# Optimization experiments

Measured on AMD Instinct MI355X. Metric: run time of the kernel, lower is better.

Reference implementation:

```python
import jax, jax.numpy as jnp
import numpy as np

H = 1024
NH = 16
HD = H // NH  # 64


def setup_inputs() -> dict:
    key = jax.random.key(0)
    ks = jax.random.split(key, 8)
    B, S = 4, 1024
    scale = 1.0 / np.sqrt(H)
    return {
        "hidden_states": jax.random.normal(ks[0], (B, S, H), jnp.float32),
        "attention_mask": jnp.ones((B, S), jnp.float32),
        "Wq": jax.random.normal(ks[1], (H, H), jnp.float32) * scale,
        "bq": jnp.zeros((H,), jnp.float32),
        "Wk": jax.random.normal(ks[2], (H, H), jnp.float32) * scale,
        "bk": jnp.zeros((H,), jnp.float32),
        "Wv": jax.random.normal(ks[3], (H, H), jnp.float32) * scale,
        "bv": jnp.zeros((H,), jnp.float32),
        "Wo": jax.random.normal(ks[4], (H, H), jnp.float32) * scale,
        "bo": jnp.zeros((H,), jnp.float32),
    }


def _split_heads(x):
    # [B,S,H] -> [B,NH,S,HD]
    B, S, _ = x.shape
    return x.reshape(B, S, NH, HD).transpose(0, 2, 1, 3)


def reference(hidden_states, attention_mask, Wq, bq, Wk, bk, Wv, bv, Wo, bo):
    B, S, _ = hidden_states.shape
    q = _split_heads(hidden_states @ Wq.T + bq)  # [B,NH,S,HD]
    k = _split_heads(hidden_states @ Wk.T + bk)
    v = _split_heads(hidden_states @ Wv.T + bv)
    scores = jnp.einsum("bhqd,bhkd->bhqk", q, k) / jnp.sqrt(jnp.float32(HD))
    # additive mask: (1 - mask) * -10000, broadcast [B,1,1,S]
    scores = scores + (1.0 - attention_mask)[:, None, None, :] * -10000.0
    probs = jax.nn.softmax(scores, axis=-1)  # dropout is identity at eval
    ctx = jnp.einsum("bhqk,bhkd->bhqd", probs, v)
    ctx = ctx.transpose(0, 2, 1, 3).reshape(B, S, H)
    out = ctx @ Wo.T + bo
    return (out, probs)
```

## Files before the change

kernel.cpp:

```cpp
#include <hip/hip_runtime.h>
#include <hip/hip_bf16.h>


typedef __attribute__((ext_vector_type(8))) short short8;
typedef __attribute__((ext_vector_type(4))) float f32x4;
typedef __attribute__((ext_vector_type(4))) short short4v;

#define LOG2E 1.44269504f
#define MFMA_BF16(a, b, c) __builtin_amdgcn_mfma_f32_16x16x32_bf16((a), (b), (c), 0, 0, 0)

__device__ __forceinline__ short f2bf(float x) {
    __hip_bfloat16 h = __float2bfloat16(x);
    return __builtin_bit_cast(short, h);
}
__device__ __forceinline__ float bf2f(short s) {
    __hip_bfloat16 h = __builtin_bit_cast(__hip_bfloat16, s);
    return __bfloat162float(h);
}

__device__ __forceinline__ void gload16(const void* g, void* lds) {
    __builtin_amdgcn_global_load_lds(
        (const __attribute__((address_space(1))) void*)g,
        (__attribute__((address_space(3))) void*)lds, 16, 0, 0);
}

__global__ __launch_bounds__(256) void cvt_bf16_kernel(const float* __restrict__ src,
                                                       short* __restrict__ dst, int n8) {
    int i = blockIdx.x * 256 + threadIdx.x;
    if (i >= n8) return;
    const float4* s = (const float4*)src;
    float4 a = s[i * 2], b = s[i * 2 + 1];
    short8 o;
    o[0] = f2bf(a.x); o[1] = f2bf(a.y); o[2] = f2bf(a.z); o[3] = f2bf(a.w);
    o[4] = f2bf(b.x); o[5] = f2bf(b.y); o[6] = f2bf(b.z); o[7] = f2bf(b.w);
    *(short8*)(dst + (size_t)i * 8) = o;
}

__global__ __launch_bounds__(256) void cvt4_kernel(const float* __restrict__ s0,
                                                   const float* __restrict__ s1,
                                                   const float* __restrict__ s2,
                                                   const float* __restrict__ s3,
                                                   short* __restrict__ dst) {
    int sel = blockIdx.x >> 9;
    const float* srcs[4] = {s0, s1, s2, s3};
    const float* s = srcs[sel];
    int li = (blockIdx.x & 511) * 256 + threadIdx.x;
    const float4* sp = (const float4*)s;
    float4 a = sp[li * 2], b = sp[li * 2 + 1];
    short8 o;
    o[0] = f2bf(a.x); o[1] = f2bf(a.y); o[2] = f2bf(a.z); o[3] = f2bf(a.w);
    o[4] = f2bf(b.x); o[5] = f2bf(b.y); o[6] = f2bf(b.z); o[7] = f2bf(b.w);
    *(short8*)(dst + ((size_t)sel * 131072 + li) * 8) = o;
}

template <int EPI>
__global__ __launch_bounds__(256) void gemm128_kernel(
    const short* __restrict__ A, const short* __restrict__ B,
    float* __restrict__ Cf, const float* __restrict__ bias0,
    short* __restrict__ qhi, short* __restrict__ qlo,
    short* __restrict__ khi, short* __restrict__ klo, short* __restrict__ vt,
    const float* __restrict__ biasq, const float* __restrict__ biask,
    const float* __restrict__ biasv)
{
    __shared__ short smem[16384];
    int tid = threadIdx.x;
    int l = tid & 63, w = tid >> 6;
    int lr = l & 15, lg = l >> 4;
    int wm = w >> 1, wn = w & 1;
    int m0 = blockIdx.y * 128, n0 = blockIdx.x * 128;

    f32x4 acc[4][4] = {};

    int sr = l >> 2;
    int sc = (l & 3) * 16;
    const char* Ag = (const char*)A + ((size_t)(m0 + w * 32 + sr) * 1024) * 2 + sc;
    const char* Bg = (const char*)B + ((size_t)(n0 + w * 32 + sr) * 1024) * 2 + sc;

    auto stage = [&](int buf, int t) {
        int kb = t * 64;
        #pragma unroll
        for (int g = 0; g < 2; ++g) {
            gload16(Ag + (size_t)g * (16 * 2048) + kb,
                    (char*)&smem[buf * 4096 + (w * 32 + g * 16) * 32]);
            gload16(Bg + (size_t)g * (16 * 2048) + kb,
                    (char*)&smem[8192 + buf * 4096 + (w * 32 + g * 16) * 32]);
        }
    };

    stage(0, 0);
    __syncthreads();

    int cur = 0;
    for (int t = 0; t < 32; ++t) {
        if (t < 31) stage(cur ^ 1, t + 1);
        short8 a[4], b[4];
        #pragma unroll
        for (int i = 0; i < 4; ++i)
            a[i] = *(const short8*)&smem[cur * 4096 + (wm * 64 + i * 16 + lr) * 32 + lg * 8];
        #pragma unroll
        for (int j = 0; j < 4; ++j)
            b[j] = *(const short8*)&smem[8192 + cur * 4096 + (wn * 64 + j * 16 + lr) * 32 + lg * 8];
        #pragma unroll
        for (int i = 0; i < 4; ++i)
            #pragma unroll
            for (int j = 0; j < 4; ++j)
                acc[i][j] = MFMA_BF16(a[i], b[j], acc[i][j]);
        __syncthreads();
        cur ^= 1;
    }

    if (EPI == 0) {
        #pragma unroll
        for (int i = 0; i < 4; ++i) {
            int m_base = m0 + wm * 64 + i * 16 + lg * 4;
            #pragma unroll
            for (int j = 0; j < 4; ++j) {
                int n = n0 + wn * 64 + j * 16 + lr;
                float bv = bias0[n];
                #pragma unroll
                for (int r = 0; r < 4; ++r)
                    Cf[(size_t)(m_base + r) * 1024 + n] = acc[i][j][r] + bv;
            }
        }
    } else {
        int sel = n0 >> 10;
        int nb = n0 & 1023;
        if (sel == 2) {
            #pragma unroll
            for (int i = 0; i < 4; ++i) {
                int ml = wm * 64 + i * 16 + lg * 4;
                #pragma unroll
                for (int j = 0; j < 4; ++j) {
                    int nl = wn * 64 + j * 16 + lr;
                    float bvv = biasv[nb + nl];
                    short4v o;
                    #pragma unroll
                    for (int r = 0; r < 4; ++r) o[r] = f2bf(acc[i][j][r] + bvv);
                    *(short4v*)((char*)smem + nl * 256 + ((ml * 2) ^ ((nl & 7) << 4))) = o;
                }
            }
            __syncthreads();
            int b_ = m0 >> 10, s0 = m0 & 1023;
            #pragma unroll
            for (int it = 0; it < 8; ++it) {
                int idx = it * 256 + tid;
                int nrow = idx >> 4, c8 = idx & 15;
                short8 vv = *(const short8*)((char*)smem + nrow * 256 +
                                             ((c8 * 16) ^ ((nrow & 7) << 4)));
                int ng = nb + nrow;
                int h = ng >> 6, d = ng & 63;
                *(short8*)(vt + (size_t)((b_ * 16 + h) * 64 + d) * 1024 + s0 + c8 * 8) = vv;
            }
        } else {
            short* Chi = sel ? khi : qhi;
            short* Clo = sel ? klo : qlo;
            const float* bias = sel ? biask : biasq;
            float ps = sel ? 1.0f : 0.125f;
            #pragma unroll
            for (int hv = 0; hv < 2; ++hv) {
                __syncthreads();
                #pragma unroll
                for (int i = 0; i < 4; ++i) {
                    int ml = wm * 64 + i * 16 + lg * 4;
                    #pragma unroll
                    for (int j = 0; j < 4; ++j) {
                        int nl = wn * 64 + j * 16 + lr;
                        float bvv = bias[nb + nl];
                        #pragma unroll
                        for (int r = 0; r < 4; ++r) {
                            float v = (acc[i][j][r] + bvv) * ps;
                            short hh = f2bf(v);
                            short ss = hv ? f2bf(v - bf2f(hh)) : hh;
                            smem[(ml + r) * 128 + nl] = ss;
                        }
                    }
                }
                __syncthreads();
                short* dst = hv ? Clo : Chi;
                #pragma unroll
                for (int it = 0; it < 8; ++it) {
                    int idx = it * 256 + tid;
                    int row = idx >> 4, c8 = idx & 15;
                    short8 vv = *(const short8*)&smem[row * 128 + c8 * 8];
                    *(short8*)(dst + (size_t)(m0 + row) * 1024 + nb + c8 * 8) = vv;
                }
            }
        }
    }
}

__global__ __launch_bounds__(256) void attn_fused_kernel(
    const short* __restrict__ Qhi, const short* __restrict__ Qlo,
    const short* __restrict__ Khi, const short* __restrict__ Klo,
    const float* __restrict__ mask, float* __restrict__ P,
    const short* __restrict__ vt, short* __restrict__ ctxb)
{
    constexpr int P_O = 0, WRM_O = 65536, WRL_O = 66048;
    __shared__ __align__(16) char lds[66560];

    int tid = threadIdx.x;
    int l = tid & 63, w = tid >> 6;
    int c = l & 15, g = l >> 4;
    int z = blockIdx.y;
    int b = z >> 4, h = z & 15;
    int qb = blockIdx.x;

    short8 bqh[2][2], bql[2][2];
    #pragma unroll
    for (int qt = 0; qt < 2; ++qt) {
        int row = qt * 16 + c;
        #pragma unroll
        for (int dt = 0; dt < 2; ++dt) {
            size_t gq = ((size_t)(b * 1024 + qb * 32 + row)) * 1024 + h * 64 + (dt * 4 + g) * 8;
            bqh[qt][dt] = *(const short8*)(Qhi + gq);
            bql[qt][dt] = *(const short8*)(Qlo + gq);
        }
    }
    asm volatile("s_waitcnt vmcnt(0)" ::: "memory");

    auto stageK = [&](int buf, int cc) {
        int r0 = w * 32;
        #pragma unroll
        for (int i = 0; i < 4; ++i) {
            int r_ = r0 + i * 8 + (l >> 3);
            int ul = (l & 7) ^ (r_ & 7);
            size_t gk = ((size_t)(b * 1024 + cc * 128 + r_)) * 1024 + h * 64 + ul * 8;
            gload16(Khi + gk, lds + buf * 32768 + (r0 + i * 8) * 128);
            gload16(Klo + gk, lds + buf * 32768 + 16384 + (r0 + i * 8) * 128);
        }
    };

    f32x4 acc[8][2][2] = {};

    stageK(0, 0);
    #pragma unroll
    for (int cc = 0; cc < 8; ++cc) {
        if (cc < 7) {
            stageK((cc + 1) & 1, cc + 1);
            asm volatile("s_waitcnt vmcnt(8)" ::: "memory");
        } else {
            asm volatile("s_waitcnt vmcnt(0)" ::: "memory");
        }
        __builtin_amdgcn_sched_barrier(0);
        const char* kb = lds + (cc & 1) * 32768;
        #pragma unroll
        for (int kt = 0; kt < 2; ++kt) {
            int row = w * 32 + kt * 16 + c;
            #pragma unroll
            for (int dt = 0; dt < 2; ++dt) {
                int u = (dt * 4 + g) ^ (row & 7);
                short8 ah = *(const short8*)(kb + row * 128 + u * 16);
                short8 al = *(const short8*)(kb + 16384 + row * 128 + u * 16);
                #pragma unroll
                for (int qt = 0; qt < 2; ++qt) {
                    acc[cc][kt][qt] = MFMA_BF16(ah, bqh[qt][dt], acc[cc][kt][qt]);
                    acc[cc][kt][qt] = MFMA_BF16(ah, bql[qt][dt], acc[cc][kt][qt]);
                    acc[cc][kt][qt] = MFMA_BF16(al, bqh[qt][dt], acc[cc][kt][qt]);
                }
            }
        }
    }

    const float* mrow = mask + b * 1024;
    float mx[2] = {-3.0e38f, -3.0e38f};
    #pragma unroll
    for (int cc = 0; cc < 8; ++cc)
        #pragma unroll
        for (int kt = 0; kt < 2; ++kt) {
            int k = cc * 128 + w * 32 + kt * 16 + g * 4;
            float4 mm = *(const float4*)(mrow + k);
            f32x4 md;
            md[0] = (1.0f - mm.x) * -10000.0f;
            md[1] = (1.0f - mm.y) * -10000.0f;
            md[2] = (1.0f - mm.z) * -10000.0f;
            md[3] = (1.0f - mm.w) * -10000.0f;
            #pragma unroll
            for (int qt = 0; qt < 2; ++qt) {
                f32x4 v = acc[cc][kt][qt] + md;
                acc[cc][kt][qt] = v;
                mx[qt] = fmaxf(mx[qt], fmaxf(fmaxf(v[0], v[1]), fmaxf(v[2], v[3])));
            }
        }
    #pragma unroll
    for (int qt = 0; qt < 2; ++qt) {
        mx[qt] = fmaxf(mx[qt], __shfl_xor(mx[qt], 16));
        mx[qt] = fmaxf(mx[qt], __shfl_xor(mx[qt], 32));
    }
    float* wrm = (float*)(lds + WRM_O);
    float* wrl = (float*)(lds + WRL_O);
    if (g == 0) { wrm[w * 32 + c] = mx[0]; wrm[w * 32 + 16 + c] = mx[1]; }
    __syncthreads();
    float mfin[2];
    mfin[0] = fmaxf(fmaxf(wrm[c], wrm[32 + c]), fmaxf(wrm[64 + c], wrm[96 + c]));
    mfin[1] = fmaxf(fmaxf(wrm[16 + c], wrm[48 + c]), fmaxf(wrm[80 + c], wrm[112 + c]));

    float sum[2] = {0.0f, 0.0f};
    #pragma unroll
    for (int cc = 0; cc < 8; ++cc)
        #pragma unroll
        for (int kt = 0; kt < 2; ++kt)
            #pragma unroll
            for (int qt = 0; qt < 2; ++qt) {
                f32x4 v = acc[cc][kt][qt];
                v[0] = exp2f((v[0] - mfin[qt]) * LOG2E);
                v[1] = exp2f((v[1] - mfin[qt]) * LOG2E);
                v[2] = exp2f((v[2] - mfin[qt]) * LOG2E);
                v[3] = exp2f((v[3] - mfin[qt]) * LOG2E);
                acc[cc][kt][qt] = v;
                sum[qt] += (v[0] + v[1]) + (v[2] + v[3]);
            }
    #pragma unroll
    for (int qt = 0; qt < 2; ++qt) {
        sum[qt] += __shfl_xor(sum[qt], 16);
        sum[qt] += __shfl_xor(sum[qt], 32);
    }
    if (g == 0) { wrl[w * 32 + c] = sum[0]; wrl[w * 32 + 16 + c] = sum[1]; }
    __syncthreads();
    float inv[2];
    inv[0] = 1.0f / ((wrl[c] + wrl[32 + c]) + (wrl[64 + c] + wrl[96 + c]));
    inv[1] = 1.0f / ((wrl[16 + c] + wrl[48 + c]) + (wrl[80 + c] + wrl[112 + c]));

    float* Pz = P + ((size_t)z << 20);
    #pragma unroll
    for (int cc = 0; cc < 8; ++cc)
        #pragma unroll
        for (int kt = 0; kt < 2; ++kt)
            #pragma unroll
            for (int qt = 0; qt < 2; ++qt) {
                f32x4 v = acc[cc][kt][qt];
                v[0] *= inv[qt]; v[1] *= inv[qt]; v[2] *= inv[qt]; v[3] *= inv[qt];
                int q = qt * 16 + c;
                int k = cc * 128 + w * 32 + kt * 16 + g * 4;
                *(f32x4*)(Pz + (size_t)(qb * 32 + q) * 1024 + k) = v;
                short4v ps4;
                ps4[0] = f2bf(v[0]); ps4[1] = f2bf(v[1]);
                ps4[2] = f2bf(v[2]); ps4[3] = f2bf(v[3]);
                *(short4v*)(lds + P_O + q * 2048 + ((k * 2) ^ ((q & 7) << 4))) = ps4;
            }
    __syncthreads();

    {
        const short* vbase = vt + (size_t)z * 65536 + (size_t)(w * 16 + c) * 1024 + g * 8;
        f32x4 pacc[2] = {};
        short8 vfrag = *(const short8*)vbase;
        for (int kc = 0; kc < 32; ++kc) {
            short8 vnext = {};
            if (kc < 31) vnext = *(const short8*)(vbase + (kc + 1) * 32);
            short8 pa[2];
            #pragma unroll
            for (int qt = 0; qt < 2; ++qt) {
                int q = qt * 16 + c;
                int kbyte = kc * 64 + g * 16;
                pa[qt] = *(const short8*)(lds + P_O + q * 2048 + (kbyte ^ ((q & 7) << 4)));
            }
            pacc[0] = MFMA_BF16(pa[0], vfrag, pacc[0]);
            pacc[1] = MFMA_BF16(pa[1], vfrag, pacc[1]);
            vfrag = vnext;
        }
        #pragma unroll
        for (int qt = 0; qt < 2; ++qt) {
            int s = qb * 32 + qt * 16 + g * 4;
            size_t base = ((size_t)b * 1024 + s) * 1024 + h * 64 + w * 16 + c;
            #pragma unroll
            for (int r = 0; r < 4; ++r)
                ctxb[base + (size_t)r * 1024] = f2bf(pacc[qt][r]);
        }
    }
}

extern "C" void kernel_launch(void* const* d_in, const int* in_sizes, int n_in,
                              void* d_out, int out_size, void* d_ws, size_t ws_size,
                              hipStream_t stream) {
    const float* hs   = (const float*)d_in[0];
    const float* mask = (const float*)d_in[1];
    const float* Wq   = (const float*)d_in[2];
    const float* bq   = (const float*)d_in[3];
    const float* Wk   = (const float*)d_in[4];
    const float* bk   = (const float*)d_in[5];
    const float* Wv   = (const float*)d_in[6];
    const float* bv   = (const float*)d_in[7];
    const float* Wo   = (const float*)d_in[8];
    const float* bo   = (const float*)d_in[9];

    float* out   = (float*)d_out;
    float* probs = out + 4194304;

    char* ws = (char*)d_ws;
    short* qhi  = (short*)(ws);
    short* qlo  = (short*)(ws + (8u << 20));
    short* khi  = (short*)(ws + (16u << 20));
    short* klo  = (short*)(ws + (24u << 20));
    short* vt   = (short*)(ws + (32u << 20));
    short* ctxb = (short*)(ws + (40u << 20));
    short* hsb  = (short*)(ws + (48u << 20));
    short* wcat = (short*)(ws + (56u << 20));
    short* wob  = wcat + 3 * (1u << 20);

    dim3 blk(256);

    cvt_bf16_kernel<<<2048, blk, 0, stream>>>(hs, hsb, 524288);
    cvt4_kernel<<<2048, blk, 0, stream>>>(Wq, Wk, Wv, Wo, wcat);

    gemm128_kernel<1><<<dim3(24, 32), blk, 0, stream>>>(
        hsb, wcat, nullptr, nullptr, qhi, qlo, khi, klo, vt, bq, bk, bv);

    attn_fused_kernel<<<dim3(32, 64), blk, 0, stream>>>(qhi, qlo, khi, klo, mask, probs,
                                                        vt, ctxb);

    gemm128_kernel<0><<<dim3(8, 32), blk, 0, stream>>>(
        ctxb, wob, out, bo, nullptr, nullptr, nullptr, nullptr, nullptr,
        nullptr, nullptr, nullptr);
}
```

Baseline: 246.8 us.

## Restage probability and context stores through LDS, remap blocks, single-buffer K

The attention kernel now writes the probability matrix in a second pass. It reads the bf16 P tile back from LDS and emits full-row coalesced nontemporal float4 stores, replacing the scattered per-fragment fp32 stores. The context output is also staged in LDS so it can go out as 16-byte row stores. The launch becomes a 1D grid with an XCD-aware block index remap. K staging drops double buffering in favour of a single buffer with barriers. The stored probabilities are now bf16-rounded values widened back to fp32, which loses precision, and the removed K prefetch may expose load latency.

Result: slower. 712.5 us, median of 2 (+188.6%).

```diff
diff --git a/kernel.cpp b/kernel.cpp
--- a/kernel.cpp
+++ b/kernel.cpp
@@ -14,8 +14,8 @@
     return __builtin_bit_cast(short, h);
 }
 __device__ __forceinline__ float bf2f(short s) {
-    __hip_bfloat16 h = __builtin_bit_cast(__hip_bfloat16, s);
-    return __bfloat162float(h);
+    unsigned int u = ((unsigned int)(unsigned short)s) << 16;
+    return __builtin_bit_cast(float, u);
 }
 
 __device__ __forceinline__ void gload16(const void* g, void* lds) {
@@ -195,15 +195,19 @@
     const float* __restrict__ mask, float* __restrict__ P,
     const short* __restrict__ vt, short* __restrict__ ctxb)
 {
-    constexpr int P_O = 0, WRM_O = 65536, WRL_O = 66048;
-    __shared__ __align__(16) char lds[66560];
+    constexpr int P_O = 0, KHI_O = 0, KLO_O = 16384,
+                  WRM_O = 65536, WRL_O = 66048, CTX_O = 66560;
+    __shared__ __align__(16) char lds[70656];
 
     int tid = threadIdx.x;
     int l = tid & 63, w = tid >> 6;
     int c = l & 15, g = l >> 4;
-    int z = blockIdx.y;
+
+    int hw = blockIdx.x;
+    int logical = (hw & 7) * 256 + (hw >> 3);
+    int z = logical >> 5;
+    int qb = logical & 31;
     int b = z >> 4, h = z & 15;
-    int qb = blockIdx.x;
 
     short8 bqh[2][2], bql[2][2];
     #pragma unroll
@@ -216,41 +220,30 @@
             bql[qt][dt] = *(const short8*)(Qlo + gq);
         }
     }
-    asm volatile("s_waitcnt vmcnt(0)" ::: "memory");
-
-    auto stageK = [&](int buf, int cc) {
-        int r0 = w * 32;
+
+    f32x4 acc[8][2][2] = {};
+
+    #pragma unroll 1
+    for (int cc = 0; cc < 8; ++cc) {
         #pragma unroll
         for (int i = 0; i < 4; ++i) {
-            int r_ = r0 + i * 8 + (l >> 3);
+            int r_ = i * 32 + w * 8 + (l >> 3);
             int ul = (l & 7) ^ (r_ & 7);
             size_t gk = ((size_t)(b * 1024 + cc * 128 + r_)) * 1024 + h * 64 + ul * 8;
-            gload16(Khi + gk, lds + buf * 32768 + (r0 + i * 8) * 128);
-            gload16(Klo + gk, lds + buf * 32768 + 16384 + (r0 + i * 8) * 128);
-        }
-    };
-
-    f32x4 acc[8][2][2] = {};
-
-    stageK(0, 0);
-    #pragma unroll
-    for (int cc = 0; cc < 8; ++cc) {
-        if (cc < 7) {
-            stageK((cc + 1) & 1, cc + 1);
-            asm volatile("s_waitcnt vmcnt(8)" ::: "memory");
-        } else {
-            asm volatile("s_waitcnt vmcnt(0)" ::: "memory");
-        }
-        __builtin_amdgcn_sched_barrier(0);
-        const char* kb = lds + (cc & 1) * 32768;
+            gload16(Khi + gk, lds + KHI_O + i * 4096 + w * 1024);
+            gload16(Klo + gk, lds + KLO_O + i * 4096 + w * 1024);
+        }
+        asm volatile("s_waitcnt vmcnt(0)" ::: "memory");
+        __syncthreads();
+
         #pragma unroll
         for (int kt = 0; kt < 2; ++kt) {
             int row = w * 32 + kt * 16 + c;
             #pragma unroll
             for (int dt = 0; dt < 2; ++dt) {
                 int u = (dt * 4 + g) ^ (row & 7);
-                short8 ah = *(const short8*)(kb + row * 128 + u * 16);
-                short8 al = *(const short8*)(kb + 16384 + row * 128 + u * 16);
+                short8 ah = *(const short8*)(lds + KHI_O + row * 128 + u * 16);
+                short8 al = *(const short8*)(lds + KLO_O + row * 128 + u * 16);
                 #pragma unroll
                 for (int qt = 0; qt < 2; ++qt) {
                     acc[cc][kt][qt] = MFMA_BF16(ah, bqh[qt][dt], acc[cc][kt][qt]);
@@ -259,6 +252,7 @@
                 }
             }
         }
+        __syncthreads();
     }
 
     const float* mrow = mask + b * 1024;
@@ -320,7 +314,6 @@
     inv[0] = 1.0f / ((wrl[c] + wrl[32 + c]) + (wrl[64 + c] + wrl[96 + c]));
     inv[1] = 1.0f / ((wrl[16 + c] + wrl[48 + c]) + (wrl[80 + c] + wrl[112 + c]));
 
-    float* Pz = P + ((size_t)z << 20);
     #pragma unroll
     for (int cc = 0; cc < 8; ++cc)
         #pragma unroll
@@ -331,13 +324,34 @@
                 v[0] *= inv[qt]; v[1] *= inv[qt]; v[2] *= inv[qt]; v[3] *= inv[qt];
                 int q = qt * 16 + c;
                 int k = cc * 128 + w * 32 + kt * 16 + g * 4;
-                *(f32x4*)(Pz + (size_t)(qb * 32 + q) * 1024 + k) = v;
                 short4v ps4;
                 ps4[0] = f2bf(v[0]); ps4[1] = f2bf(v[1]);
                 ps4[2] = f2bf(v[2]); ps4[3] = f2bf(v[3]);
                 *(short4v*)(lds + P_O + q * 2048 + ((k * 2) ^ ((q & 7) << 4))) = ps4;
             }
     __syncthreads();
+
+    {
+        float* Pz = P + ((size_t)z << 20) + (size_t)(qb * 32) * 1024;
+        #pragma unroll
+        for (int rr = 0; rr < 8; ++rr) {
+            int q = w * 8 + rr;
+            int swz = (q & 7) << 4;
+            int kb = l * 32;
+            short8 s0 = *(const short8*)(lds + P_O + q * 2048 + (kb ^ swz));
+            short8 s1 = *(const short8*)(lds + P_O + q * 2048 + ((kb + 16) ^ swz));
+            float* dst = Pz + (size_t)q * 1024 + l * 16;
+            f32x4 o;
+            o[0] = bf2f(s0[0]); o[1] = bf2f(s0[1]); o[2] = bf2f(s0[2]); o[3] = bf2f(s0[3]);
+            __builtin_nontemporal_store(o, (f32x4*)dst);
+            o[0] = bf2f(s0[4]); o[1] = bf2f(s0[5]); o[2] = bf2f(s0[6]); o[3] = bf2f(s0[7]);
+            __builtin_nontemporal_store(o, (f32x4*)(dst + 4));
+            o[0] = bf2f(s1[0]); o[1] = bf2f(s1[1]); o[2] = bf2f(s1[2]); o[3] = bf2f(s1[3]);
+            __builtin_nontemporal_store(o, (f32x4*)(dst + 8));
+            o[0] = bf2f(s1[4]); o[1] = bf2f(s1[5]); o[2] = bf2f(s1[6]); o[3] = bf2f(s1[7]);
+            __builtin_nontemporal_store(o, (f32x4*)(dst + 12));
+        }
+    }
 
     {
         const short* vbase = vt + (size_t)z * 65536 + (size_t)(w * 16 + c) * 1024 + g * 8;
@@ -357,14 +371,20 @@
             pacc[1] = MFMA_BF16(pa[1], vfrag, pacc[1]);
             vfrag = vnext;
         }
-        #pragma unroll
-        for (int qt = 0; qt < 2; ++qt) {
-            int s = qb * 32 + qt * 16 + g * 4;
-            size_t base = ((size_t)b * 1024 + s) * 1024 + h * 64 + w * 16 + c;
+        short* cl = (short*)(lds + CTX_O);
+        #pragma unroll
+        for (int qt = 0; qt < 2; ++qt)
             #pragma unroll
             for (int r = 0; r < 4; ++r)
-                ctxb[base + (size_t)r * 1024] = f2bf(pacc[qt][r]);
-        }
+                cl[(qt * 16 + g * 4 + r) * 64 + w * 16 + c] = f2bf(pacc[qt][r]);
+    }
+    __syncthreads();
+
+    {
+        const short* cl = (const short*)(lds + CTX_O);
+        int q = tid >> 3, dc = tid & 7;
+        short8 vv = *(const short8*)(cl + q * 64 + dc * 8);
+        *(short8*)(ctxb + ((size_t)(b * 1024 + qb * 32 + q)) * 1024 + h * 64 + dc * 8) = vv;
     }
 }
 
@@ -404,8 +424,8 @@
     gemm128_kernel<1><<<dim3(24, 32), blk, 0, stream>>>(
         hsb, wcat, nullptr, nullptr, qhi, qlo, khi, klo, vt, bq, bk, bv);
 
-    attn_fused_kernel<<<dim3(32, 64), blk, 0, stream>>>(qhi, qlo, khi, klo, mask, probs,
-                                                        vt, ctxb);
+    attn_fused_kernel<<<2048, blk, 0, stream>>>(qhi, qlo, khi, klo, mask, probs,
+                                                vt, ctxb);
 
     gemm128_kernel<0><<<dim3(8, 32), blk, 0, stream>>>(
         ctxb, wob, out, bo, nullptr, nullptr, nullptr, nullptr, nullptr,
```
